# Kernel optimization log

Hardware: AMD Instinct MI355X
Metric: run time of the kernel (lower is better)

The kernel has to match this reference:

```python
import jax, jax.numpy as jnp
import numpy as np

BETA = 0.25
N_E = 4096
E_DIM = 64
B, T = 16, 1024


def setup_inputs() -> dict:
    key = jax.random.key(0)
    k1, k2 = jax.random.split(key)
    z = jax.random.normal(k1, (B, T, E_DIM), dtype=jnp.float32)
    # embedding.weight.data.uniform_(-1/n_e, 1/n_e)
    codebook = jax.random.uniform(k2, (N_E, E_DIM), dtype=jnp.float32,
                                  minval=-1.0 / N_E, maxval=1.0 / N_E)
    return {"z": z, "codebook": codebook}


def reference(z, codebook):
    # z: (B, T, e_dim), codebook: (n_e, e_dim)
    n_e, e_dim = codebook.shape
    zf = z.reshape(-1, e_dim)  # (N, e_dim)

    # d[n, k] = ||z_n||^2 + ||e_k||^2 - 2 z_n . e_k   -> (N, n_e)
    d = (jnp.sum(zf * zf, axis=1, keepdims=True)
         + jnp.sum(codebook * codebook, axis=1)
         - 2.0 * jnp.matmul(zf, codebook.T))

    idx = jnp.argmin(d, axis=1)                  # (N,) int
    z_q = codebook[idx].reshape(z.shape)         # (B, T, e_dim)

    sg = jax.lax.stop_gradient
    loss = jnp.mean((z_q - sg(z)) ** 2) + BETA * jnp.mean((sg(z_q) - z) ** 2)

    # straight-through estimator
    z_q_st = z + sg(z_q - z)

    # e_mean = mean over tokens of one-hot encodings == normalized code counts
    n_tokens = idx.shape[0]
    counts = jnp.zeros((n_e,), dtype=z.dtype).at[idx].add(1.0)
    e_mean = counts / n_tokens
    perplexity = jnp.exp(-jnp.sum(e_mean * jnp.log(e_mean + 1e-10)))

    return (loss, z_q_st, idx, perplexity)
```

## Files before the change

### kernel.cpp

```cpp
#include <hip/hip_runtime.h>
#include <math.h>

#define N_TOK   16384
#define EDIM    64
#define NE      4096
#define NSLICE  16
#define CSLICE  (NE / NSLICE)
#define CHUNK   128
#define TPB     256
#define TOKPT   2
#define ZQ_OFF  1
#define IDX_OFF (1 + N_TOK * EDIM)
#define PERP_OFF (IDX_OFF + N_TOK)

typedef unsigned long long u64;

__global__ __launch_bounds__(256) void norms_zero_kernel(
    const float* __restrict__ z, const float* __restrict__ cb,
    float* __restrict__ nz, float* __restrict__ ne,
    int* __restrict__ hist, float* __restrict__ lossAcc) {
#pragma clang fp contract(off)
    int i = blockIdx.x * 256 + threadIdx.x;
    if (i < NE) hist[i] = 0;
    if (i == 0) lossAcc[0] = 0.0f;
    const float* row;
    float* dst;
    if (i < N_TOK)            { row = z  + (size_t)i * EDIM;           dst = nz + i; }
    else if (i < N_TOK + NE)  { row = cb + (size_t)(i - N_TOK) * EDIM; dst = ne + (i - N_TOK); }
    else return;

    float r[8];
#pragma unroll
    for (int j = 0; j < 8; ++j) { float v = row[j]; r[j] = v * v; }
#pragma unroll
    for (int b = 8; b < 64; b += 8) {
#pragma unroll
        for (int j = 0; j < 8; ++j) { float v = row[b + j]; r[j] = r[j] + v * v; }
    }
    dst[0] = ((r[0] + r[1]) + (r[2] + r[3])) + ((r[4] + r[5]) + (r[6] + r[7]));
}

__global__ __launch_bounds__(256, 2) void dist_argmin_kernel(
    const float* __restrict__ z, const float* __restrict__ cb,
    const float* __restrict__ nz, const float* __restrict__ ne,
    u64* __restrict__ part) {
    __shared__ float se[CHUNK * EDIM];
    __shared__ float sne[CHUNK];
    const int tid    = threadIdx.x;
    const int token0 = blockIdx.x * (TPB * TOKPT) + tid;
    const int token1 = token0 + TPB;
    const int slice  = blockIdx.y;

    float zr0[EDIM], zr1[EDIM];
    {
        const float4* zp0 = (const float4*)(z + (size_t)token0 * EDIM);
        const float4* zp1 = (const float4*)(z + (size_t)token1 * EDIM);
#pragma unroll
        for (int j = 0; j < 16; ++j) {
            float4 v = zp0[j];
            zr0[4 * j + 0] = v.x; zr0[4 * j + 1] = v.y;
            zr0[4 * j + 2] = v.z; zr0[4 * j + 3] = v.w;
            float4 w = zp1[j];
            zr1[4 * j + 0] = w.x; zr1[4 * j + 1] = w.y;
            zr1[4 * j + 2] = w.z; zr1[4 * j + 3] = w.w;
        }
    }
    const float tnz0 = nz[token0];
    const float tnz1 = nz[token1];
    u64 best0 = ~0ull, best1 = ~0ull;

#pragma unroll 1
    for (int c = 0; c < CSLICE / CHUNK; ++c) {
        const int kbase = slice * CSLICE + c * CHUNK;
        {
            const float4* src = (const float4*)(cb + (size_t)kbase * EDIM);
            float4* dst = (float4*)se;
#pragma unroll
            for (int r = 0; r < (CHUNK * EDIM / 4) / TPB; ++r)
                dst[r * TPB + tid] = src[r * TPB + tid];
            if (tid < CHUNK / 4)
                ((float4*)sne)[tid] = ((const float4*)(ne + kbase))[tid];
        }
        __syncthreads();

#pragma unroll 1
        for (int k = 0; k < CHUNK; k += 2) {
            const float4* e0 = (const float4*)(se + (size_t)(k + 0) * EDIM);
            const float4* e1 = (const float4*)(se + (size_t)(k + 1) * EDIM);
            float d00 = 0.f, d01 = 0.f, d10 = 0.f, d11 = 0.f;
#pragma unroll
            for (int q = 0; q < 16; ++q) {
                float4 a = e0[q];
                float4 b = e1[q];
                d00 = __builtin_fmaf(zr0[4 * q + 0], a.x, d00);
                d00 = __builtin_fmaf(zr0[4 * q + 1], a.y, d00);
                d00 = __builtin_fmaf(zr0[4 * q + 2], a.z, d00);
                d00 = __builtin_fmaf(zr0[4 * q + 3], a.w, d00);
                d01 = __builtin_fmaf(zr0[4 * q + 0], b.x, d01);
                d01 = __builtin_fmaf(zr0[4 * q + 1], b.y, d01);
                d01 = __builtin_fmaf(zr0[4 * q + 2], b.z, d01);
                d01 = __builtin_fmaf(zr0[4 * q + 3], b.w, d01);
                d10 = __builtin_fmaf(zr1[4 * q + 0], a.x, d10);
                d10 = __builtin_fmaf(zr1[4 * q + 1], a.y, d10);
                d10 = __builtin_fmaf(zr1[4 * q + 2], a.z, d10);
                d10 = __builtin_fmaf(zr1[4 * q + 3], a.w, d10);
                d11 = __builtin_fmaf(zr1[4 * q + 0], b.x, d11);
                d11 = __builtin_fmaf(zr1[4 * q + 1], b.y, d11);
                d11 = __builtin_fmaf(zr1[4 * q + 2], b.z, d11);
                d11 = __builtin_fmaf(zr1[4 * q + 3], b.w, d11);
            }
            const float s0 = sne[k + 0], s1 = sne[k + 1];
            float t00 = __builtin_fmaf(-2.0f, d00, tnz0 + s0);
            float t01 = __builtin_fmaf(-2.0f, d01, tnz0 + s1);
            float t10 = __builtin_fmaf(-2.0f, d10, tnz1 + s0);
            float t11 = __builtin_fmaf(-2.0f, d11, tnz1 + s1);
            u64 p;
            p = ((u64)__float_as_uint(t00) << 32) | (u64)(kbase + k + 0); if (p < best0) best0 = p;
            p = ((u64)__float_as_uint(t01) << 32) | (u64)(kbase + k + 1); if (p < best0) best0 = p;
            p = ((u64)__float_as_uint(t10) << 32) | (u64)(kbase + k + 0); if (p < best1) best1 = p;
            p = ((u64)__float_as_uint(t11) << 32) | (u64)(kbase + k + 1); if (p < best1) best1 = p;
        }
        __syncthreads();
    }
    part[(size_t)slice * N_TOK + token0] = best0;
    part[(size_t)slice * N_TOK + token1] = best1;
}

__global__ __launch_bounds__(256) void reduce_gather_kernel(
    const float* __restrict__ z, const float* __restrict__ cb,
    const u64* __restrict__ part, int* __restrict__ hist,
    float* __restrict__ lossAcc, float* __restrict__ out) {
    const int t = blockIdx.x * 256 + threadIdx.x;
    u64 best = part[t];
#pragma unroll
    for (int s = 1; s < NSLICE; ++s) {
        u64 p = part[(size_t)s * N_TOK + t];
        if (p < best) best = p;
    }
    const int idx = (int)(best & 0xFFFFFFFFull);
    out[IDX_OFF + t] = (float)idx;
    atomicAdd(&hist[idx], 1);

    const float4* ev = (const float4*)(cb + (size_t)idx * EDIM);
    const float4* zv = (const float4*)(z + (size_t)t * EDIM);
    float* o = out + ZQ_OFF + (size_t)t * EDIM;
    float acc = 0.0f;
#pragma unroll
    for (int j = 0; j < 16; ++j) {
        float4 e = ev[j], zz = zv[j];
        float d;
        d = e.x - zz.x; o[4 * j + 0] = zz.x + d; acc = __builtin_fmaf(d, d, acc);
        d = e.y - zz.y; o[4 * j + 1] = zz.y + d; acc = __builtin_fmaf(d, d, acc);
        d = e.z - zz.z; o[4 * j + 2] = zz.z + d; acc = __builtin_fmaf(d, d, acc);
        d = e.w - zz.w; o[4 * j + 3] = zz.w + d; acc = __builtin_fmaf(d, d, acc);
    }
    __shared__ float red[256];
    red[threadIdx.x] = acc;
    __syncthreads();
    for (int s = 128; s > 0; s >>= 1) {
        if (threadIdx.x < s) red[threadIdx.x] += red[threadIdx.x + s];
        __syncthreads();
    }
    if (threadIdx.x == 0) atomicAdd(lossAcc, red[0]);
}

__global__ __launch_bounds__(256) void finalize_kernel(
    const int* __restrict__ hist, const float* __restrict__ lossAcc,
    float* __restrict__ out) {
    __shared__ float red[256];
    float acc = 0.0f;
    for (int i = threadIdx.x; i < NE; i += 256) {
        float e = (float)hist[i] * (1.0f / 16384.0f);
        acc += e * logf(e + 1e-10f);
    }
    red[threadIdx.x] = acc;
    __syncthreads();
    for (int s = 128; s > 0; s >>= 1) {
        if (threadIdx.x < s) red[threadIdx.x] += red[threadIdx.x + s];
        __syncthreads();
    }
    if (threadIdx.x == 0) {
        out[PERP_OFF] = expf(-red[0]);
        float m = lossAcc[0] * (1.0f / 1048576.0f);
        out[0] = m + 0.25f * m;
    }
}

extern "C" void kernel_launch(void* const* d_in, const int* in_sizes, int n_in,
                              void* d_out, int out_size, void* d_ws, size_t ws_size,
                              hipStream_t stream) {
    const float* z  = (const float*)d_in[0];
    const float* cb = (const float*)d_in[1];
    float* out = (float*)d_out;

    char* ws = (char*)d_ws;
    u64*   part    = (u64*)ws;
    float* nz      = (float*)(ws + (size_t)NSLICE * N_TOK * 8);
    float* ne      = nz + N_TOK;
    int*   hist    = (int*)(ne + NE);
    float* lossAcc = (float*)(hist + NE);

    hipLaunchKernelGGL(norms_zero_kernel, dim3(80), dim3(256), 0, stream,
                       z, cb, nz, ne, hist, lossAcc);
    hipLaunchKernelGGL(dist_argmin_kernel,
                       dim3(N_TOK / (TPB * TOKPT), NSLICE), dim3(TPB), 0, stream,
                       z, cb, nz, ne, part);
    hipLaunchKernelGGL(reduce_gather_kernel, dim3(64), dim3(256), 0, stream,
                       z, cb, part, hist, lossAcc, out);
    hipLaunchKernelGGL(finalize_kernel, dim3(1), dim3(256), 0, stream,
                       hist, lossAcc, out);
}
```

Baseline: 198.7 us.

## Rewrite distance kernel as 8x8 register-tiled outer product with swizzled LDS tiles

```diff
diff --git a/kernel.cpp b/kernel.cpp
--- a/kernel.cpp
+++ b/kernel.cpp
@@ -5,10 +5,7 @@
 #define EDIM    64
 #define NE      4096
 #define NSLICE  16
-#define CSLICE  (NE / NSLICE)
-#define CHUNK   128
 #define TPB     256
-#define TOKPT   2
 #define ZQ_OFF  1
 #define IDX_OFF (1 + N_TOK * EDIM)
 #define PERP_OFF (IDX_OFF + N_TOK)
@@ -44,86 +41,111 @@
     const float* __restrict__ z, const float* __restrict__ cb,
     const float* __restrict__ nz, const float* __restrict__ ne,
     u64* __restrict__ part) {
-    __shared__ float se[CHUNK * EDIM];
-    __shared__ float sne[CHUNK];
-    const int tid    = threadIdx.x;
-    const int token0 = blockIdx.x * (TPB * TOKPT) + tid;
-    const int token1 = token0 + TPB;
-    const int slice  = blockIdx.y;
-
-    float zr0[EDIM], zr1[EDIM];
+    __shared__ float4 zt[2048];
+    __shared__ float4 ct[2048];
+    const int tid   = threadIdx.x;
+    const int tg    = tid & 15;
+    const int cg    = tid >> 4;
+    const int bx    = blockIdx.x;
+    const int slice = blockIdx.y;
+    const int tok0  = bx * 128;
+
     {
-        const float4* zp0 = (const float4*)(z + (size_t)token0 * EDIM);
-        const float4* zp1 = (const float4*)(z + (size_t)token1 * EDIM);
-#pragma unroll
-        for (int j = 0; j < 16; ++j) {
-            float4 v = zp0[j];
-            zr0[4 * j + 0] = v.x; zr0[4 * j + 1] = v.y;
-            zr0[4 * j + 2] = v.z; zr0[4 * j + 3] = v.w;
-            float4 w = zp1[j];
-            zr1[4 * j + 0] = w.x; zr1[4 * j + 1] = w.y;
-            zr1[4 * j + 2] = w.z; zr1[4 * j + 3] = w.w;
-        }
-    }
-    const float tnz0 = nz[token0];
-    const float tnz1 = nz[token1];
-    u64 best0 = ~0ull, best1 = ~0ull;
+        const float4* zp = (const float4*)z + (size_t)tok0 * 16;
+#pragma unroll
+        for (int r = 0; r < 8; ++r) {
+            const int f   = tid * 8 + r;
+            const int tl  = f >> 4;
+            const int q   = f & 15;
+            const int row = q * 8 + (tl & 7);
+            const int col = (tl >> 3) ^ (row & 15);
+            zt[row * 16 + col] = zp[f];
+        }
+    }
+
+    float tnz[8];
+#pragma unroll
+    for (int i = 0; i < 8; ++i) tnz[i] = nz[tok0 + tg * 8 + i];
+
+    u64 best[8];
+#pragma unroll
+    for (int i = 0; i < 8; ++i) best[i] = ~0ull;
 
 #pragma unroll 1
-    for (int c = 0; c < CSLICE / CHUNK; ++c) {
-        const int kbase = slice * CSLICE + c * CHUNK;
+    for (int c = 0; c < 2; ++c) {
+        const int kbase = slice * 256 + c * 128;
         {
-            const float4* src = (const float4*)(cb + (size_t)kbase * EDIM);
-            float4* dst = (float4*)se;
-#pragma unroll
-            for (int r = 0; r < (CHUNK * EDIM / 4) / TPB; ++r)
-                dst[r * TPB + tid] = src[r * TPB + tid];
-            if (tid < CHUNK / 4)
-                ((float4*)sne)[tid] = ((const float4*)(ne + kbase))[tid];
-        }
-        __syncthreads();
-
-#pragma unroll 1
-        for (int k = 0; k < CHUNK; k += 2) {
-            const float4* e0 = (const float4*)(se + (size_t)(k + 0) * EDIM);
-            const float4* e1 = (const float4*)(se + (size_t)(k + 1) * EDIM);
-            float d00 = 0.f, d01 = 0.f, d10 = 0.f, d11 = 0.f;
-#pragma unroll
-            for (int q = 0; q < 16; ++q) {
-                float4 a = e0[q];
-                float4 b = e1[q];
-                d00 = __builtin_fmaf(zr0[4 * q + 0], a.x, d00);
-                d00 = __builtin_fmaf(zr0[4 * q + 1], a.y, d00);
-                d00 = __builtin_fmaf(zr0[4 * q + 2], a.z, d00);
-                d00 = __builtin_fmaf(zr0[4 * q + 3], a.w, d00);
-                d01 = __builtin_fmaf(zr0[4 * q + 0], b.x, d01);
-                d01 = __builtin_fmaf(zr0[4 * q + 1], b.y, d01);
-                d01 = __builtin_fmaf(zr0[4 * q + 2], b.z, d01);
-                d01 = __builtin_fmaf(zr0[4 * q + 3], b.w, d01);
-                d10 = __builtin_fmaf(zr1[4 * q + 0], a.x, d10);
-                d10 = __builtin_fmaf(zr1[4 * q + 1], a.y, d10);
-                d10 = __builtin_fmaf(zr1[4 * q + 2], a.z, d10);
-                d10 = __builtin_fmaf(zr1[4 * q + 3], a.w, d10);
-                d11 = __builtin_fmaf(zr1[4 * q + 0], b.x, d11);
-                d11 = __builtin_fmaf(zr1[4 * q + 1], b.y, d11);
-                d11 = __builtin_fmaf(zr1[4 * q + 2], b.z, d11);
-                d11 = __builtin_fmaf(zr1[4 * q + 3], b.w, d11);
-            }
-            const float s0 = sne[k + 0], s1 = sne[k + 1];
-            float t00 = __builtin_fmaf(-2.0f, d00, tnz0 + s0);
-            float t01 = __builtin_fmaf(-2.0f, d01, tnz0 + s1);
-            float t10 = __builtin_fmaf(-2.0f, d10, tnz1 + s0);
-            float t11 = __builtin_fmaf(-2.0f, d11, tnz1 + s1);
-            u64 p;
-            p = ((u64)__float_as_uint(t00) << 32) | (u64)(kbase + k + 0); if (p < best0) best0 = p;
-            p = ((u64)__float_as_uint(t01) << 32) | (u64)(kbase + k + 1); if (p < best0) best0 = p;
-            p = ((u64)__float_as_uint(t10) << 32) | (u64)(kbase + k + 0); if (p < best1) best1 = p;
-            p = ((u64)__float_as_uint(t11) << 32) | (u64)(kbase + k + 1); if (p < best1) best1 = p;
-        }
-        __syncthreads();
-    }
-    part[(size_t)slice * N_TOK + token0] = best0;
-    part[(size_t)slice * N_TOK + token1] = best1;
+            const float4* cp = (const float4*)cb + (size_t)kbase * 16;
+#pragma unroll
+            for (int r = 0; r < 8; ++r) {
+                const int f   = tid * 8 + r;
+                const int lc  = f >> 4;
+                const int q   = f & 15;
+                const int row = q * 8 + (lc & 7);
+                const int col = (lc >> 3) ^ (row & 15);
+                ct[row * 16 + col] = cp[f];
+            }
+        }
+        float sne[8];
+#pragma unroll
+        for (int j = 0; j < 8; ++j) sne[j] = ne[kbase + cg * 8 + j];
+        __syncthreads();
+
+        float acc[8][8];
+#pragma unroll
+        for (int i = 0; i < 8; ++i)
+#pragma unroll
+            for (int j = 0; j < 8; ++j) acc[i][j] = 0.0f;
+
+#pragma unroll
+        for (int q = 0; q < 16; ++q) {
+            float4 zf[8], cf[8];
+#pragma unroll
+            for (int i = 0; i < 8; ++i) {
+                const int row = q * 8 + i;
+                zf[i] = zt[row * 16 + (tg ^ (row & 15))];
+            }
+#pragma unroll
+            for (int j = 0; j < 8; ++j) {
+                const int row = q * 8 + j;
+                cf[j] = ct[row * 16 + (cg ^ (row & 15))];
+            }
+#pragma unroll
+            for (int i = 0; i < 8; ++i)
+#pragma unroll
+                for (int j = 0; j < 8; ++j) {
+                    acc[i][j] = __builtin_fmaf(zf[i].x, cf[j].x, acc[i][j]);
+                    acc[i][j] = __builtin_fmaf(zf[i].y, cf[j].y, acc[i][j]);
+                    acc[i][j] = __builtin_fmaf(zf[i].z, cf[j].z, acc[i][j]);
+                    acc[i][j] = __builtin_fmaf(zf[i].w, cf[j].w, acc[i][j]);
+                }
+        }
+
+#pragma unroll
+        for (int i = 0; i < 8; ++i)
+#pragma unroll
+            for (int j = 0; j < 8; ++j) {
+                const float d = __builtin_fmaf(-2.0f, acc[i][j], tnz[i] + sne[j]);
+                const u64 p = ((u64)__float_as_uint(d) << 32)
+                            | (u64)(kbase + cg * 8 + j);
+                if (p < best[i]) best[i] = p;
+            }
+        __syncthreads();
+    }
+
+    u64* red = (u64*)ct;
+#pragma unroll
+    for (int i = 0; i < 8; ++i) red[cg * 128 + tg * 8 + i] = best[i];
+    __syncthreads();
+    if (tid < 128) {
+        u64 b = red[tid];
+#pragma unroll
+        for (int s = 1; s < 16; ++s) {
+            const u64 p = red[s * 128 + tid];
+            if (p < b) b = p;
+        }
+        part[(size_t)slice * N_TOK + tok0 + tid] = b;
+    }
 }
 
 __global__ __launch_bounds__(256) void reduce_gather_kernel(
@@ -203,7 +225,7 @@
     hipLaunchKernelGGL(norms_zero_kernel, dim3(80), dim3(256), 0, stream,
                        z, cb, nz, ne, hist, lossAcc);
     hipLaunchKernelGGL(dist_argmin_kernel,
-                       dim3(N_TOK / (TPB * TOKPT), NSLICE), dim3(TPB), 0, stream,
+                       dim3(N_TOK / 128, NSLICE), dim3(TPB), 0, stream,
                        z, cb, nz, ne, part);
     hipLaunchKernelGGL(reduce_gather_kernel, dim3(64), dim3(256), 0, stream,
                        z, cb, part, hist, lossAcc, out);
```

Result: no change. 195.5 us (-1.6%).
